# Optimization experiments

Measured on AMD Instinct MI355X. Metric: run time of the kernel, lower is better.

## Reference

```python
import jax, jax.numpy as jnp
import numpy as np

D_MODEL = 1024
N_HEADS = 16
D_K = D_MODEL // N_HEADS
B, S = 2, 2048


def setup_inputs() -> dict:
    key = jax.random.key(0)
    ks = jax.random.split(key, 12)
    s = 1.0 / np.sqrt(D_MODEL)
    inp = {
        "query": jax.random.normal(ks[0], (B, S, D_MODEL), jnp.float32),
        "key": jax.random.normal(ks[1], (B, S, D_MODEL), jnp.float32),
        "value": jax.random.normal(ks[2], (B, S, D_MODEL), jnp.float32),
        "W_q": jax.random.uniform(ks[3], (D_MODEL, D_MODEL), jnp.float32, -s, s),
        "b_q": jnp.zeros((D_MODEL,), jnp.float32),
        "W_k": jax.random.uniform(ks[4], (D_MODEL, D_MODEL), jnp.float32, -s, s),
        "b_k": jnp.zeros((D_MODEL,), jnp.float32),
        "W_v": jax.random.uniform(ks[5], (D_MODEL, D_MODEL), jnp.float32, -s, s),
        "b_v": jnp.zeros((D_MODEL,), jnp.float32),
        "W_o": jax.random.uniform(ks[6], (D_MODEL, D_MODEL), jnp.float32, -s, s),
        "b_o": jnp.zeros((D_MODEL,), jnp.float32),
        "ln_gamma": jnp.ones((D_MODEL,), jnp.float32),
        "ln_beta": jnp.zeros((D_MODEL,), jnp.float32),
    }
    return inp


def _layer_norm(x, gamma, beta, eps=1e-5):
    mu = jnp.mean(x, axis=-1, keepdims=True)
    var = jnp.var(x, axis=-1, keepdims=True)
    return (x - mu) * jax.lax.rsqrt(var + eps) * gamma + beta


def reference(query, key, value, W_q, b_q, W_k, b_k, W_v, b_v, W_o, b_o, ln_gamma, ln_beta):
    b, s, _ = query.shape
    # projections -> [b, h, s, d_k]
    q = (query @ W_q.T + b_q).reshape(b, s, N_HEADS, D_K).transpose(0, 2, 1, 3)
    k = (key @ W_k.T + b_k).reshape(b, s, N_HEADS, D_K).transpose(0, 2, 1, 3)
    v = (value @ W_v.T + b_v).reshape(b, s, N_HEADS, D_K).transpose(0, 2, 1, 3)
    # scaled dot-product attention (no mask)
    scores = jnp.einsum('bhqd,bhkd->bhqk', q, k) / jnp.sqrt(jnp.float32(D_K))
    attn = jax.nn.softmax(scores, axis=-1)
    ctx = jnp.einsum('bhqk,bhkd->bhqd', attn, v)  # [b,h,s,d_k]
    ctx = ctx.transpose(0, 2, 1, 3).reshape(b, s, D_MODEL)
    out = ctx @ W_o.T + b_o
    # residual uses the PROJECTED query (quirk of original module); dropout=identity (eval)
    resid = q.transpose(0, 2, 1, 3).reshape(b, s, D_MODEL)
    return _layer_norm(out + resid, ln_gamma, ln_beta)
```

## Files before the change

kernel.cpp:

```cpp
#include <hip/hip_runtime.h>

#define DM 1024
#define NH 16
#define DKq 64
#define BB 2
#define SS 2048
#define MTOT 4096

#define K2f 0.18033688011112042f
#define IK2f 5.545177444479562f

typedef __attribute__((ext_vector_type(4))) float f32x4;
typedef __attribute__((ext_vector_type(16))) float f32x16;
typedef __attribute__((ext_vector_type(8))) short s16x8;
typedef __attribute__((ext_vector_type(4))) short s16x4;
typedef __attribute__((ext_vector_type(4))) unsigned short u16x4;

__device__ __forceinline__ unsigned short f2bf(float f) {
    unsigned u = __float_as_uint(f);
    u += 0x7fff + ((u >> 16) & 1);
    return (unsigned short)(u >> 16);
}

__device__ __forceinline__ float bf2f(unsigned short x) {
    return __uint_as_float((unsigned)x << 16);
}

__device__ __forceinline__ s16x8 cvt8(f32x4 a, f32x4 b) {
    s16x8 r;
    r[0] = (short)f2bf(a[0]); r[1] = (short)f2bf(a[1]);
    r[2] = (short)f2bf(a[2]); r[3] = (short)f2bf(a[3]);
    r[4] = (short)f2bf(b[0]); r[5] = (short)f2bf(b[1]);
    r[6] = (short)f2bf(b[2]); r[7] = (short)f2bf(b[3]);
    return r;
}

__device__ __forceinline__ unsigned pkp(float a, float b) {
    return __builtin_amdgcn_perm(__float_as_uint(b), __float_as_uint(a), 0x07060302u);
}

__device__ __forceinline__ void gload_lds16(const void* g, void* l) {
    __builtin_amdgcn_global_load_lds(
        (const __attribute__((address_space(1))) unsigned int*)g,
        (__attribute__((address_space(3))) unsigned int*)l,
        16, 0, 0);
}

__global__ __launch_bounds__(256)
void cvt_kernel(const float* __restrict__ s0, const float* __restrict__ s1,
                const float* __restrict__ s2, const float* __restrict__ s3,
                const float* __restrict__ s4, const float* __restrict__ s5,
                const float* __restrict__ s6,
                unsigned short* __restrict__ Xb, unsigned short* __restrict__ Wb)
{
    const int seg = blockIdx.y;
    const float* src;
    unsigned short* dst;
    int n;
    if (seg < 3) {
        src = (seg == 0) ? s0 : (seg == 1) ? s1 : s2;
        dst = Xb + (size_t)seg * (MTOT * DM);
        n = MTOT * DM;
    } else {
        src = (seg == 3) ? s3 : (seg == 4) ? s4 : (seg == 5) ? s5 : s6;
        dst = Wb + (size_t)(seg - 3) * (DM * DM);
        n = DM * DM;
    }
    const int stride = gridDim.x * 256;
    for (int i = blockIdx.x * 256 + threadIdx.x; i * 8 < n; i += stride) {
        f32x4 a = *(const f32x4*)(src + (size_t)i * 8);
        f32x4 b = *(const f32x4*)(src + (size_t)i * 8 + 4);
        *(s16x8*)(dst + (size_t)i * 8) = cvt8(a, b);
    }
}

__global__ __launch_bounds__(256)
void proj_kernel(const unsigned short* __restrict__ Xb,
                 const unsigned short* __restrict__ Wb,
                 const float* __restrict__ bq, const float* __restrict__ bk,
                 const float* __restrict__ bv,
                 unsigned short* __restrict__ Qh, unsigned short* __restrict__ Kh,
                 unsigned short* __restrict__ Vt)
{
    const int z = blockIdx.z;
    const unsigned short* X = Xb + (size_t)z * (MTOT * DM);
    const unsigned short* W = Wb + (size_t)z * (DM * DM);
    const float* bias = (z == 0) ? bq : (z == 1) ? bk : bv;

    const int m0 = blockIdx.y * 128;
    const int n0 = blockIdx.x * 128;
    const int tid  = threadIdx.x;
    const int lane = tid & 63;
    const int w    = tid >> 6;
    const int wm   = w >> 1, wn = w & 1;

    __shared__ __align__(16) short lA[128 * 64];
    __shared__ __align__(16) short lB[128 * 64];

    f32x4 acc[4][4];
#pragma unroll
    for (int i = 0; i < 4; i++)
#pragma unroll
        for (int j = 0; j < 4; j++) acc[i][j] = (f32x4)(0.f);

    const int lrow = lane >> 3;
    const int lcg  = (lane & 7) ^ lrow;

    for (int kt = 0; kt < 16; ++kt) {
        const int k0 = kt * 64;
#pragma unroll
        for (int p = 0; p < 4; ++p) {
            int c = w * 4 + p;
            int row = c * 8 + lrow;
            gload_lds16(X + (size_t)(m0 + row) * DM + k0 + lcg * 8,
                        (char*)lA + c * 1024);
            gload_lds16(W + (size_t)(n0 + row) * DM + k0 + lcg * 8,
                        (char*)lB + c * 1024);
        }
        __syncthreads();
#pragma unroll
        for (int kk = 0; kk < 2; ++kk) {
            s16x8 af[4], bf[4];
#pragma unroll
            for (int i = 0; i < 4; i++) {
                int row = wm * 64 + i * 16 + (lane & 15);
                int byte = (kk * 64 + 16 * (lane >> 4)) ^ ((row & 7) << 4);
                af[i] = *(const s16x8*)((const char*)lA + row * 128 + byte);
            }
#pragma unroll
            for (int i = 0; i < 4; i++) {
                int row = wn * 64 + i * 16 + (lane & 15);
                int byte = (kk * 64 + 16 * (lane >> 4)) ^ ((row & 7) << 4);
                bf[i] = *(const s16x8*)((const char*)lB + row * 128 + byte);
            }
#pragma unroll
            for (int i = 0; i < 4; i++)
#pragma unroll
                for (int j = 0; j < 4; j++)
                    acc[i][j] = __builtin_amdgcn_mfma_f32_16x16x32_bf16(
                        af[i], bf[j], acc[i][j], 0, 0, 0);
        }
        __syncthreads();
    }

#pragma unroll
    for (int i = 0; i < 4; i++) {
#pragma unroll
        for (int j = 0; j < 4; j++) {
            int rg0 = m0 + wm * 64 + i * 16 + 4 * (lane >> 4);
            int cg  = n0 + wn * 64 + j * 16 + (lane & 15);
            int b = rg0 >> 11, s0 = rg0 & 2047, h = cg >> 6, d = cg & 63;
            float bv_ = bias[cg];
            if (z == 2) {
                int s0p = (s0 & ~12) | ((s0 & 4) << 1) | ((s0 & 8) >> 1);
                u16x4 st;
#pragma unroll
                for (int e = 0; e < 4; e++) st[e] = f2bf(acc[i][j][e] + bv_);
                *(u16x4*)&Vt[(((size_t)(b * NH + h)) * DKq + d) * SS + s0p] = st;
            } else if (z == 0) {
#pragma unroll
                for (int e = 0; e < 4; e++)
                    Qh[(((size_t)(b * NH + h)) * SS + s0 + e) * DKq + d] =
                        f2bf((acc[i][j][e] + bv_) * K2f);
            } else {
#pragma unroll
                for (int e = 0; e < 4; e++)
                    Kh[(((size_t)(b * NH + h)) * SS + s0 + e) * DKq + d] =
                        f2bf(acc[i][j][e] + bv_);
            }
        }
    }
}

__device__ __forceinline__ void attn_tile32(
    const char* __restrict__ lkc, const char* __restrict__ lvc,
    const s16x8* aq, s16x8 onesv, int l31, int hi,
    f32x16& o0, f32x16& o1, f32x16& o4)
{
    f32x16 s0 = (f32x16)(0.f), s1 = (f32x16)(0.f);
    const int sw = (l31 & 7) << 4;
    __builtin_amdgcn_s_setprio(1);
#pragma unroll
    for (int kkd = 0; kkd < 4; kkd++) {
        const int byte = (32 * kkd + 16 * hi) ^ sw;
        s16x8 ak0 = *(const s16x8*)(lkc + l31 * 128 + byte);
        s0 = __builtin_amdgcn_mfma_f32_32x32x16_bf16(ak0, aq[kkd], s0, 0, 0, 0);
        s16x8 ak1 = *(const s16x8*)(lkc + (32 + l31) * 128 + byte);
        s1 = __builtin_amdgcn_mfma_f32_32x32x16_bf16(ak1, aq[kkd], s1, 0, 0, 0);
    }
    __builtin_amdgcn_s_setprio(0);

#pragma unroll
    for (int r = 0; r < 16; r++) {
        s0[r] = __builtin_amdgcn_exp2f(s0[r]);
        s1[r] = __builtin_amdgcn_exp2f(s1[r]);
    }

    __builtin_amdgcn_s_setprio(1);
#pragma unroll
    for (int jb = 0; jb < 2; jb++) {
#pragma unroll
        for (int u = 0; u < 2; u++) {
            const int t = 2 * jb + u;
            union { unsigned uu[4]; s16x8 v; } bp;
            if (jb == 0) {
                bp.uu[0] = pkp(s0[8*u+0], s0[8*u+1]);
                bp.uu[1] = pkp(s0[8*u+2], s0[8*u+3]);
                bp.uu[2] = pkp(s0[8*u+4], s0[8*u+5]);
                bp.uu[3] = pkp(s0[8*u+6], s0[8*u+7]);
            } else {
                bp.uu[0] = pkp(s1[8*u+0], s1[8*u+1]);
                bp.uu[1] = pkp(s1[8*u+2], s1[8*u+3]);
                bp.uu[2] = pkp(s1[8*u+4], s1[8*u+5]);
                bp.uu[3] = pkp(s1[8*u+6], s1[8*u+7]);
            }
            const int vbyte = (32 * t + 16 * hi) ^ sw;
            s16x8 av0 = *(const s16x8*)(lvc + l31 * 128 + vbyte);
            o0 = __builtin_amdgcn_mfma_f32_32x32x16_bf16(av0, bp.v, o0, 0, 0, 0);
            s16x8 av1 = *(const s16x8*)(lvc + (32 + l31) * 128 + vbyte);
            o1 = __builtin_amdgcn_mfma_f32_32x32x16_bf16(av1, bp.v, o1, 0, 0, 0);
            o4 = __builtin_amdgcn_mfma_f32_32x32x16_bf16(onesv, bp.v, o4, 0, 0, 0);
        }
    }
    __builtin_amdgcn_s_setprio(0);
}

__global__ __launch_bounds__(256)
void attn_kernel(const unsigned short* __restrict__ Qh,
                 const unsigned short* __restrict__ Kh,
                 const unsigned short* __restrict__ Vt,
                 unsigned short* __restrict__ Ctx)
{
    const int bh = blockIdx.y;
    const int q0 = blockIdx.x * 128;
    const int tid = threadIdx.x, lane = tid & 63, w = tid >> 6;
    const int b = bh >> 4, h = bh & 15;
    const int l31 = lane & 31;
    const int hi  = lane >> 5;

    __shared__ __align__(16) short lKs[2][64 * 64];
    __shared__ __align__(16) short lVs[2][64 * 64];

    const size_t qk_base = (size_t)bh * SS * DKq;
    const size_t vt_base = (size_t)bh * DKq * SS;

    s16x8 aq[4];
    const int qrow = q0 + 32 * w + l31;
    {
        const unsigned short* qp = Qh + qk_base + (size_t)qrow * DKq + 8 * hi;
#pragma unroll
        for (int kkd = 0; kkd < 4; kkd++)
            aq[kkd] = *(const s16x8*)(qp + 16 * kkd);
    }

    s16x8 onesv;
#pragma unroll
    for (int i = 0; i < 8; i++) onesv[i] = (short)0x3F80;

    f32x16 o0 = (f32x16)(0.f), o1 = (f32x16)(0.f), o4 = (f32x16)(0.f);

    const int lrow = lane >> 3;
    const int lcg  = (lane & 7) ^ lrow;

#define STAGE(BUF, KV0) {                                                     \
    char* dk = (char*)lKs[BUF]; char* dv = (char*)lVs[BUF];                   \
    _Pragma("unroll")                                                         \
    for (int p = 0; p < 2; ++p) {                                             \
        int c = 2 * w + p;                                                    \
        gload_lds16(Kh + qk_base + (size_t)((KV0) + c * 8 + lrow) * DKq + lcg * 8, \
                    dk + c * 1024);                                           \
        gload_lds16(Vt + vt_base + (size_t)(c * 8 + lrow) * SS + (KV0) + lcg * 8,  \
                    dv + c * 1024);                                           \
    } }

    STAGE(0, 0);
    __syncthreads();

    for (int th = 0; th < 16; ++th) {
        const int t0 = th * 2;
        STAGE(1, (t0 + 1) * 64);
        attn_tile32((const char*)lKs[0], (const char*)lVs[0], aq, onesv, l31, hi, o0, o1, o4);
        __syncthreads();
        if (t0 + 2 < 32) STAGE(0, (t0 + 2) * 64);
        attn_tile32((const char*)lKs[1], (const char*)lVs[1], aq, onesv, l31, hi, o0, o1, o4);
        __syncthreads();
    }
#undef STAGE

    const float inv = 1.0f / o4[0];
    unsigned short* crow = Ctx + ((size_t)(b * SS + qrow)) * DM + h * 64;
#pragma unroll
    for (int db = 0; db < 2; db++) {
#pragma unroll
        for (int v = 0; v < 4; v++) {
            u16x4 st;
#pragma unroll
            for (int e = 0; e < 4; e++) {
                float x = (db == 0) ? o0[4 * v + e] : o1[4 * v + e];
                st[e] = f2bf(x * inv);
            }
            *(u16x4*)(crow + 32 * db + 8 * v + 4 * hi) = st;
        }
    }
}

__global__ __launch_bounds__(256)
void outproj_kernel(const unsigned short* __restrict__ Ctx,
                    const unsigned short* __restrict__ Wo,
                    const float* __restrict__ bo,
                    const unsigned short* __restrict__ Qh,
                    float* __restrict__ Out)
{
    const int m0 = blockIdx.y * 128;
    const int n0 = blockIdx.x * 128;
    const int tid = threadIdx.x, lane = tid & 63, w = tid >> 6;
    const int wm = w >> 1, wn = w & 1;

    __shared__ __align__(16) short lA[128 * 64];
    __shared__ __align__(16) short lB[128 * 64];

    f32x4 acc[4][4];
#pragma unroll
    for (int i = 0; i < 4; i++)
#pragma unroll
        for (int j = 0; j < 4; j++) acc[i][j] = (f32x4)(0.f);

    const int lrow = lane >> 3;
    const int lcg  = (lane & 7) ^ lrow;

    for (int kt = 0; kt < 16; ++kt) {
        const int k0 = kt * 64;
#pragma unroll
        for (int p = 0; p < 4; ++p) {
            int c = w * 4 + p;
            int row = c * 8 + lrow;
            gload_lds16(Ctx + (size_t)(m0 + row) * DM + k0 + lcg * 8,
                        (char*)lA + c * 1024);
            gload_lds16(Wo + (size_t)(n0 + row) * DM + k0 + lcg * 8,
                        (char*)lB + c * 1024);
        }
        __syncthreads();
#pragma unroll
        for (int kk = 0; kk < 2; ++kk) {
            s16x8 af[4], bf[4];
#pragma unroll
            for (int i = 0; i < 4; i++) {
                int row = wm * 64 + i * 16 + (lane & 15);
                int byte = (kk * 64 + 16 * (lane >> 4)) ^ ((row & 7) << 4);
                af[i] = *(const s16x8*)((const char*)lA + row * 128 + byte);
            }
#pragma unroll
            for (int i = 0; i < 4; i++) {
                int row = wn * 64 + i * 16 + (lane & 15);
                int byte = (kk * 64 + 16 * (lane >> 4)) ^ ((row & 7) << 4);
                bf[i] = *(const s16x8*)((const char*)lB + row * 128 + byte);
            }
#pragma unroll
            for (int i = 0; i < 4; i++)
#pragma unroll
                for (int j = 0; j < 4; j++)
                    acc[i][j] = __builtin_amdgcn_mfma_f32_16x16x32_bf16(
                        af[i], bf[j], acc[i][j], 0, 0, 0);
        }
        __syncthreads();
    }

#pragma unroll
    for (int i = 0; i < 4; i++) {
#pragma unroll
        for (int j = 0; j < 4; j++) {
            int rg0 = m0 + wm * 64 + i * 16 + 4 * (lane >> 4);
            int cg  = n0 + wn * 64 + j * 16 + (lane & 15);
            int b = rg0 >> 11, s0 = rg0 & 2047, h = cg >> 6, d = cg & 63;
            float bo_ = bo[cg];
#pragma unroll
            for (int e = 0; e < 4; e++) {
                float res = bf2f(Qh[(((size_t)(b * NH + h)) * SS + s0 + e) * DKq + d]);
                Out[(size_t)(rg0 + e) * DM + cg] =
                    __builtin_fmaf(res, IK2f, acc[i][j][e] + bo_);
            }
        }
    }
}

__global__ __launch_bounds__(256)
void ln_kernel(float* __restrict__ Out, const float* __restrict__ gamma,
               const float* __restrict__ beta)
{
    const int row = blockIdx.x;
    float* rp = Out + (size_t)row * DM;
    const int tid = threadIdx.x;

    f32x4 x = *(const f32x4*)(rp + tid * 4);
    float s  = x[0] + x[1] + x[2] + x[3];
    float sq = x[0] * x[0] + x[1] * x[1] + x[2] * x[2] + x[3] * x[3];
#pragma unroll
    for (int off = 1; off < 64; off <<= 1) {
        s  += __shfl_xor(s, off);
        sq += __shfl_xor(sq, off);
    }
    __shared__ float ps[4], pq[4];
    const int w = tid >> 6;
    if ((tid & 63) == 0) { ps[w] = s; pq[w] = sq; }
    __syncthreads();
    float ts = ps[0] + ps[1] + ps[2] + ps[3];
    float tq = pq[0] + pq[1] + pq[2] + pq[3];
    float mu  = ts * (1.f / 1024.f);
    float var = tq * (1.f / 1024.f) - mu * mu;
    float rst = rsqrtf(var + 1e-5f);

    f32x4 g  = *(const f32x4*)(gamma + tid * 4);
    f32x4 bt = *(const f32x4*)(beta + tid * 4);
    f32x4 y;
#pragma unroll
    for (int e = 0; e < 4; e++) y[e] = (x[e] - mu) * rst * g[e] + bt[e];
    *(f32x4*)(rp + tid * 4) = y;
}

extern "C" void kernel_launch(void* const* d_in, const int* in_sizes, int n_in,
                              void* d_out, int out_size, void* d_ws, size_t ws_size,
                              hipStream_t stream)
{
    const float* query = (const float*)d_in[0];
    const float* key   = (const float*)d_in[1];
    const float* value = (const float*)d_in[2];
    const float* Wq = (const float*)d_in[3];
    const float* bq = (const float*)d_in[4];
    const float* Wk = (const float*)d_in[5];
    const float* bk = (const float*)d_in[6];
    const float* Wv = (const float*)d_in[7];
    const float* bv = (const float*)d_in[8];
    const float* Wo = (const float*)d_in[9];
    const float* bo = (const float*)d_in[10];
    const float* gamma = (const float*)d_in[11];
    const float* beta  = (const float*)d_in[12];

    char* ws = (char*)d_ws;
    unsigned short* Xb  = (unsigned short*)(ws);
    unsigned short* Wb  = (unsigned short*)(ws + (24u << 20));
    unsigned short* Qh  = (unsigned short*)(ws + (32u << 20));
    unsigned short* Kh  = (unsigned short*)(ws + (40u << 20));
    unsigned short* Vt  = (unsigned short*)(ws + (48u << 20));
    unsigned short* Ctx = (unsigned short*)(ws);
    float* Out = (float*)d_out;

    cvt_kernel<<<dim3(256, 7), 256, 0, stream>>>(query, key, value,
                                                 Wq, Wk, Wv, Wo, Xb, Wb);
    proj_kernel<<<dim3(8, 32, 3), 256, 0, stream>>>(Xb, Wb, bq, bk, bv,
                                                    Qh, Kh, Vt);
    attn_kernel<<<dim3(16, 32), 256, 0, stream>>>(Qh, Kh, Vt, Ctx);
    outproj_kernel<<<dim3(8, 32), 256, 0, stream>>>(Ctx, Wb + 3u * DM * DM, bo,
                                                    Qh, Out);
    ln_kernel<<<4096, 256, 0, stream>>>(Out, gamma, beta);
}
```

Baseline: 143.8 us.

## Double-buffer LDS in projection GEMMs and remap block IDs across XCDs

```diff
diff --git a/kernel.cpp b/kernel.cpp
--- a/kernel.cpp
+++ b/kernel.cpp
@@ -40,8 +40,8 @@
 }
 
 __device__ __forceinline__ void gload_lds16(const void* g, void* l) {
-    __builtin_amdgcn_global_load_lds(
-        (const __attribute__((address_space(1))) unsigned int*)g,
+    __builtin_amdgcn_global_lo\
+ad_lds((const __attribute__((address_space(1))) unsigned int*)g,
         (__attribute__((address_space(3))) unsigned int*)l,
         16, 0, 0);
 }
@@ -82,20 +82,25 @@
                  unsigned short* __restrict__ Qh, unsigned short* __restrict__ Kh,
                  unsigned short* __restrict__ Vt)
 {
-    const int z = blockIdx.z;
+    const int bid = blockIdx.x;
+    const int t   = (bid & 7) * 96 + (bid >> 3);
+    const int z   = t >> 8;
+    const int ty  = (t >> 3) & 31;
+    const int tx  = t & 7;
+
     const unsigned short* X = Xb + (size_t)z * (MTOT * DM);
     const unsigned short* W = Wb + (size_t)z * (DM * DM);
     const float* bias = (z == 0) ? bq : (z == 1) ? bk : bv;
 
-    const int m0 = blockIdx.y * 128;
-    const int n0 = blockIdx.x * 128;
+    const int m0 = ty * 128;
+    const int n0 = tx * 128;
     const int tid  = threadIdx.x;
     const int lane = tid & 63;
     const int w    = tid >> 6;
     const int wm   = w >> 1, wn = w & 1;
 
-    __shared__ __align__(16) short lA[128 * 64];
-    __shared__ __align__(16) short lB[128 * 64];
+    __shared__ __align__(16) short lA[2][128 * 64];
+    __shared__ __align__(16) short lB[2][128 * 64];
 
     f32x4 acc[4][4];
 #pragma unroll
@@ -106,42 +111,55 @@
     const int lrow = lane >> 3;
     const int lcg  = (lane & 7) ^ lrow;
 
-    for (int kt = 0; kt < 16; ++kt) {
-        const int k0 = kt * 64;
-#pragma unroll
-        for (int p = 0; p < 4; ++p) {
-            int c = w * 4 + p;
-            int row = c * 8 + lrow;
-            gload_lds16(X + (size_t)(m0 + row) * DM + k0 + lcg * 8,
-                        (char*)lA + c * 1024);
-            gload_lds16(W + (size_t)(n0 + row) * DM + k0 + lcg * 8,
-                        (char*)lB + c * 1024);
-        }
-        __syncthreads();
-#pragma unroll
-        for (int kk = 0; kk < 2; ++kk) {
-            s16x8 af[4], bf[4];
-#pragma unroll
-            for (int i = 0; i < 4; i++) {
-                int row = wm * 64 + i * 16 + (lane & 15);
-                int byte = (kk * 64 + 16 * (lane >> 4)) ^ ((row & 7) << 4);
-                af[i] = *(const s16x8*)((const char*)lA + row * 128 + byte);
-            }
-#pragma unroll
-            for (int i = 0; i < 4; i++) {
-                int row = wn * 64 + i * 16 + (lane & 15);
-                int byte = (kk * 64 + 16 * (lane >> 4)) ^ ((row & 7) << 4);
-                bf[i] = *(const s16x8*)((const char*)lB + row * 128 + byte);
-            }
-#pragma unroll
-            for (int i = 0; i < 4; i++)
-#pragma unroll
-                for (int j = 0; j < 4; j++)
-                    acc[i][j] = __builtin_amdgcn_mfma_f32_16x16x32_bf16(
-                        af[i], bf[j], acc[i][j], 0, 0, 0);
-        }
-        __syncthreads();
-    }
+#define PSTAGE(BUF, KT) {                                                     \
+    const int k0_ = (KT) * 64;                                                \
+    _Pragma("unroll")                                                         \
+    for (int p = 0; p < 4; ++p) {                                             \
+        int c = w * 4 + p;                                                    \
+        int row = c * 8 + lrow;                                               \
+        gload_lds16(X + (size_t)(m0 + row) * DM + k0_ + lcg * 8,              \
+                    (char*)lA[BUF] + c * 1024);                               \
+        gload_lds16(W + (size_t)(n0 + row) * DM + k0_ + lcg * 8,              \
+                    (char*)lB[BUF] + c * 1024);                               \
+    } }
+
+#define PCOMPUTE(BUF) {                                                       \
+    _Pragma("unroll")                                                         \
+    for (int kk = 0; kk < 2; ++kk) {                                          \
+        s16x8 af[4], bf[4];                                                   \
+        _Pragma("unroll")                                                     \
+        for (int i = 0; i < 4; i++) {                                         \
+            int row = wm * 64 + i * 16 + (lane & 15);                         \
+            int byte = (kk * 64 + 16 * (lane >> 4)) ^ ((row & 7) << 4);       \
+            af[i] = *(const s16x8*)((const char*)lA[BUF] + row * 128 + byte); \
+        }                                                                     \
+        _Pragma("unroll")                                                     \
+        for (int i = 0; i < 4; i++) {                                         \
+            int row = wn * 64 + i * 16 + (lane & 15);                         \
+            int byte = (kk * 64 + 16 * (lane >> 4)) ^ ((row & 7) << 4);       \
+            bf[i] = *(const s16x8*)((const char*)lB[BUF] + row * 128 + byte); \
+        }                                                                     \
+        _Pragma("unroll")                                                     \
+        for (int i = 0; i < 4; i++)                                           \
+            _Pragma("unroll")                                                 \
+            for (int j = 0; j < 4; j++)                                       \
+                acc[i][j] = __builtin_amdgcn_mfma_f32_16x16x32_bf16(          \
+                    af[i], bf[j], acc[i][j], 0, 0, 0);                        \
+    } }
+
+    PSTAGE(0, 0);
+    __syncthreads();
+    for (int kh = 0; kh < 8; ++kh) {
+        const int k0 = kh * 2;
+        if (k0 + 1 < 16) PSTAGE(1, k0 + 1);
+        PCOMPUTE(0);
+        __syncthreads();
+        if (k0 + 2 < 16) PSTAGE(0, k0 + 2);
+        PCOMPUTE(1);
+        __syncthreads();
+    }
+#undef PSTAGE
+#undef PCOMPUTE
 
 #pragma unroll
     for (int i = 0; i < 4; i++) {
@@ -231,8 +249,11 @@
                  const unsigned short* __restrict__ Vt,
                  unsigned short* __restrict__ Ctx)
 {
-    const int bh = blockIdx.y;
-    const int q0 = blockIdx.x * 128;
+    const int bid = blockIdx.x;
+    const int tt  = (bid & 7) * 64 + (bid >> 3);
+    const int bh  = tt >> 4;
+    const int q0  = (tt & 15) * 128;
+
     const int tid = threadIdx.x, lane = tid & 63, w = tid >> 6;
     const int b = bh >> 4, h = bh & 15;
     const int l31 = lane & 31;
@@ -311,13 +332,18 @@
                     const unsigned short* __restrict__ Qh,
                     float* __restrict__ Out)
 {
-    const int m0 = blockIdx.y * 128;
-    const int n0 = blockIdx.x * 128;
+    const int bid = blockIdx.x;
+    const int t   = (bid & 7) * 32 + (bid >> 3);
+    const int ty  = t >> 3;
+    const int tx  = t & 7;
+
+    const int m0 = ty * 128;
+    const int n0 = tx * 128;
     const int tid = threadIdx.x, lane = tid & 63, w = tid >> 6;
     const int wm = w >> 1, wn = w & 1;
 
-    __shared__ __align__(16) short lA[128 * 64];
-    __shared__ __align__(16) short lB[128 * 64];
+    __shared__ __align__(16) short lA[2][128 * 64];
+    __shared__ __align__(16) short lB[2][128 * 64];
 
     f32x4 acc[4][4];
 #pragma unroll
@@ -328,42 +354,55 @@
     const int lrow = lane >> 3;
     const int lcg  = (lane & 7) ^ lrow;
 
-    for (int kt = 0; kt < 16; ++kt) {
-        const int k0 = kt * 64;
-#pragma unroll
-        for (int p = 0; p < 4; ++p) {
-            int c = w * 4 + p;
-            int row = c * 8 + lrow;
-            gload_lds16(Ctx + (size_t)(m0 + row) * DM + k0 + lcg * 8,
-                        (char*)lA + c * 1024);
-            gload_lds16(Wo + (size_t)(n0 + row) * DM + k0 + lcg * 8,
-                        (char*)lB + c * 1024);
-        }
-        __syncthreads();
-#pragma unroll
-        for (int kk = 0; kk < 2; ++kk) {
-            s16x8 af[4], bf[4];
-#pragma unroll
-            for (int i = 0; i < 4; i++) {
-                int row = wm * 64 + i * 16 + (lane & 15);
-                int byte = (kk * 64 + 16 * (lane >> 4)) ^ ((row & 7) << 4);
-                af[i] = *(const s16x8*)((const char*)lA + row * 128 + byte);
-            }
-#pragma unroll
-            for (int i = 0; i < 4; i++) {
-                int row = wn * 64 + i * 16 + (lane & 15);
-                int byte = (kk * 64 + 16 * (lane >> 4)) ^ ((row & 7) << 4);
-                bf[i] = *(const s16x8*)((const char*)lB + row * 128 + byte);
-            }
-#pragma unroll
-            for (int i = 0; i < 4; i++)
-#pragma unroll
-                for (int j = 0; j < 4; j++)
-                    acc[i][j] = __builtin_amdgcn_mfma_f32_16x16x32_bf16(
-                        af[i], bf[j], acc[i][j], 0, 0, 0);
-        }
-        __syncthreads();
-    }
+#define PSTAGE(BUF, KT) {                                                     \
+    const int k0_ = (KT) * 64;                                                \
+    _Pragma("unroll")                                                         \
+    for (int p = 0; p < 4; ++p) {                                             \
+        int c = w * 4 + p;                                                    \
+        int row = c * 8 + lrow;                                               \
+        gload_lds16(Ctx + (size_t)(m0 + row) * DM + k0_ + lcg * 8,            \
+                    (char*)lA[BUF] + c * 1024);                               \
+        gload_lds16(Wo + (size_t)(n0 + row) * DM + k0_ + lcg * 8,             \
+                    (char*)lB[BUF] + c * 1024);                               \
+    } }
+
+#define PCOMPUTE(BUF) {                                                       \
+    _Pragma("unroll")                                                         \
+    for (int kk = 0; kk < 2; ++kk) {                                          \
+        s16x8 af[4], bf[4];                                                   \
+        _Pragma("unroll")                                                     \
+        for (int i = 0; i < 4; i++) {                                         \
+            int row = wm * 64 + i * 16 + (lane & 15);                         \
+            int byte = (kk * 64 + 16 * (lane >> 4)) ^ ((row & 7) << 4);       \
+            af[i] = *(const s16x8*)((const char*)lA[BUF] + row * 128 + byte); \
+        }                                                                     \
+        _Pragma("unroll")                                                     \
+        for (int i = 0; i < 4; i++) {                                         \
+            int row = wn * 64 + i * 16 + (lane & 15);                         \
+            int byte = (kk * 64 + 16 * (lane >> 4)) ^ ((row & 7) << 4);       \
+            bf[i] = *(const s16x8*)((const char*)lB[BUF] + row * 128 + byte); \
+        }                                                                     \
+        _Pragma("unroll")                                                     \
+        for (int i = 0; i < 4; i++)                                           \
+            _Pragma("unroll")                                                 \
+            for (int j = 0; j < 4; j++)                                       \
+                acc[i][j] = __builtin_amdgcn_mfma_f32_16x16x32_bf16(          \
+                    af[i], bf[j], acc[i][j], 0, 0, 0);                        \
+    } }
+
+    PSTAGE(0, 0);
+    __syncthreads();
+    for (int kh = 0; kh < 8; ++kh) {
+        const int k0 = kh * 2;
+        if (k0 + 1 < 16) PSTAGE(1, k0 + 1);
+        PCOMPUTE(0);
+        __syncthreads();
+        if (k0 + 2 < 16) PSTAGE(0, k0 + 2);
+        PCOMPUTE(1);
+        __syncthreads();
+    }
+#undef PSTAGE
+#undef PCOMPUTE
 
 #pragma unroll
     for (int i = 0; i < 4; i++) {
@@ -446,10 +485,8 @@
 
     cvt_kernel<<<dim3(256, 7), 256, 0, stream>>>(query, key, value,
                                                  Wq, Wk, Wv, Wo, Xb, Wb);
-    proj_kernel<<<dim3(8, 32, 3), 256, 0, stream>>>(Xb, Wb, bq, bk, bv,
-                                                    Qh, Kh, Vt);
-    attn_kernel<<<dim3(16, 32), 256, 0, stream>>>(Qh, Kh, Vt, Ctx);
-    outproj_kernel<<<dim3(8, 32), 256, 0, stream>>>(Ctx, Wb + 3u * DM * DM, bo,
-                                                    Qh, Out);
+    proj_kernel<<<768, 256, 0, stream>>>(Xb, Wb, bq, bk, bv, Qh, Kh, Vt);
+    attn_kernel<<<512, 256, 0, stream>>>(Qh, Kh, Vt, Ctx);
+    outproj_kernel<<<256, 256, 0, stream>>>(Ctx, Wb + 3u * DM * DM, bo, Qh, Out);
     ln_kernel<<<4096, 256, 0, stream>>>(Out, gamma, beta);
 }
```

Result: faster. 140.6 us (-2.2%).
